# Optimization experiments

Hardware: AMD Instinct MI355X
Metric: run time of the kernel (lower is better)

The kernel has to match this reference:

```python
import jax, jax.numpy as jnp
import numpy as np

N, K, F, H, C = 16384, 16, 3, 64, 10


def setup_inputs() -> dict:
    key = jax.random.key(0)
    ks = jax.random.split(key, 6)
    pos = jax.random.normal(ks[0], (N, F), jnp.float32)
    batch = jnp.zeros((N,), jnp.int32)  # single graph
    W1 = jax.random.normal(ks[1], (2 * F, H), jnp.float32) * 0.1
    b1 = jnp.zeros((H,), jnp.float32)
    W2 = jax.random.normal(ks[2], (2 * H, H), jnp.float32) * 0.1
    b2 = jnp.zeros((H,), jnp.float32)
    Wc = jax.random.normal(ks[3], (H, C), jnp.float32) * 0.1
    bc = jnp.zeros((C,), jnp.float32)
    return {"pos": pos, "batch": batch, "W1": W1, "b1": b1,
            "W2": W2, "b2": b2, "Wc": Wc, "bc": bc}


def knn_graph(pos, k):
    # brute-force knn with self-loops (loop=True): self has distance 0
    sq = jnp.sum(pos * pos, axis=1)
    d = sq[:, None] + sq[None, :] - 2.0 * (pos @ pos.T)  # [N, N]
    _, idx = jax.lax.top_k(-d, k)  # [N, k] nearest neighbor indices (incl. self)
    return idx


def edge_conv(x, idx, W, b):
    # message for edge j->i: Linear(concat(x_i, x_j - x_i)); aggregate by max over neighbors
    n, k = idx.shape
    xi = x[:, None, :]               # [N, 1, F]
    xj = x[idx]                      # [N, k, F]
    msg = jnp.concatenate([jnp.broadcast_to(xi, (n, k, x.shape[1])), xj - xi], axis=-1)
    m = msg @ W + b                  # [N, k, H]
    return jnp.max(m, axis=1)        # [N, H]


def reference(pos, batch, W1, b1, W2, b2, Wc, bc):
    idx = knn_graph(pos, K)
    h = jax.nn.relu(edge_conv(pos, idx, W1, b1))
    h = jax.nn.relu(edge_conv(h, idx, W2, b2))
    g = jax.ops.segment_max(h, batch, num_segments=1)  # global max pool -> [1, H]
    return g @ Wc + bc
```

## Files before the change

kernel.cpp:

```cpp
#include <hip/hip_runtime.h>

#define NPTS 16384
#define KNN 16
#define HID 64
#define NCLS 10

#define QPB 8
#define QPW 2
#define SCAP 128

__device__ __forceinline__ float distf(float4 q, float4 p) {
    float dot = fmaf(q.x, p.x, fmaf(q.y, p.y, q.z * p.z));
    return fmaf(-2.f, dot, p.w);
}

__device__ __forceinline__ unsigned long long dkey(float v, int j) {
    unsigned u = __float_as_uint(v);
    u = (u & 0x80000000u) ? ~u : (u | 0x80000000u);
    return ((unsigned long long)u << 32) | (unsigned)j;
}

__device__ __forceinline__ unsigned long long shfl_xor_u64(unsigned long long x, int m) {
    unsigned hi = (unsigned)__shfl_xor((int)(x >> 32), m, 64);
    unsigned lo = (unsigned)__shfl_xor((int)(x & 0xffffffffu), m, 64);
    return ((unsigned long long)hi << 32) | lo;
}

__device__ __forceinline__ void wave_top16_16(unsigned long long (&key)[16], int lane,
                                              int q, int* __restrict__ idx) {
    int outj = 0x7fffffff;
    for (int r = 0; r < 16; ++r) {
        unsigned long long gm = key[0];
#pragma unroll
        for (int s = 1; s < 16; ++s) gm = key[s] < gm ? key[s] : gm;
#pragma unroll
        for (int st = 1; st < 64; st <<= 1) {
            unsigned long long o = shfl_xor_u64(gm, st);
            gm = o < gm ? o : gm;
        }
        if (lane == r) outj = (int)(gm & 0xffffffffu);
#pragma unroll
        for (int s = 0; s < 16; ++s)
            if (key[s] == gm) key[s] = ~0ull;
    }
    if (lane < 16) idx[q * KNN + lane] = outj;
}

__global__ void prep_kernel(const float* __restrict__ pos, float4* __restrict__ pos4) {
    int i = blockIdx.x * 256 + threadIdx.x;
    if (i < NPTS) {
        float x = pos[3 * i], y = pos[3 * i + 1], z = pos[3 * i + 2];
        pos4[i] = make_float4(x, y, z, fmaf(x, x, fmaf(y, y, z * z)));
    }
}

__global__ __launch_bounds__(256) void knn_kernel(const float4* __restrict__ pos4,
                                                  int* __restrict__ idx) {
    __shared__ float4 tile[256];
    __shared__ unsigned long long keys[QPB][SCAP];
    __shared__ int knt[QPB];
    int tid = threadIdx.x;
    int lane = tid & 63;
    int w = tid >> 6;
    int qb = blockIdx.x * QPB + w * QPW;
    float4 q0 = pos4[qb + 0], q1 = pos4[qb + 1];

    float m0 = INFINITY, m1 = INFINITY;
    for (int tb = 0; tb < NPTS; tb += 256) {
        __syncthreads();
        tile[tid] = pos4[tb + tid];
        __syncthreads();
#pragma unroll
        for (int r = 0; r < 4; ++r) {
            float4 p = tile[r * 64 + lane];
            m0 = fminf(m0, distf(q0, p));
            m1 = fminf(m1, distf(q1, p));
        }
    }
    m0 = fminf(m0, __shfl_xor(m0, 16, 64));
    m1 = fminf(m1, __shfl_xor(m1, 16, 64));
    m0 = fminf(m0, __shfl_xor(m0, 32, 64));
    m1 = fminf(m1, __shfl_xor(m1, 32, 64));
#pragma unroll
    for (int mk = 1; mk <= 8; mk <<= 1) {
        m0 = fmaxf(m0, __shfl_xor(m0, mk, 64));
        m1 = fmaxf(m1, __shfl_xor(m1, mk, 64));
    }
    float tq0 = m0, tq1 = m1;
    if (lane < QPW) knt[w * QPW + lane] = 0;

    for (int tb = 0; tb < NPTS; tb += 256) {
        __syncthreads();
        tile[tid] = pos4[tb + tid];
        __syncthreads();
#pragma unroll
        for (int r = 0; r < 4; ++r) {
            int jj = r * 64 + lane;
            float4 p = tile[jj];
            int j = tb + jj;
            float v0 = distf(q0, p);
            float v1 = distf(q1, p);
            if (v0 <= tq0) { int s = atomicAdd(&knt[w * QPW + 0], 1); if (s < SCAP) keys[w * QPW + 0][s] = dkey(v0, j); }
            if (v1 <= tq1) { int s = atomicAdd(&knt[w * QPW + 1], 1); if (s < SCAP) keys[w * QPW + 1][s] = dkey(v1, j); }
        }
    }

#pragma unroll
    for (int qi = 0; qi < QPW; ++qi) {
        int q = qb + qi;
        int ntot = knt[w * QPW + qi];
        if (ntot <= SCAP) {
            unsigned long long k0 = (lane < ntot) ? keys[w * QPW + qi][lane] : ~0ull;
            unsigned long long k1 = (lane + 64 < ntot) ? keys[w * QPW + qi][lane + 64] : ~0ull;
            int r0 = 0, r1 = 0;
            for (int t = 0; t < ntot; ++t) {
                unsigned long long k = keys[w * QPW + qi][t];
                r0 += (int)(k < k0);
                r1 += (int)(k < k1);
            }
            if (lane < ntot && r0 < KNN) idx[q * KNN + r0] = (int)(k0 & 0xffffffffu);
            if (lane + 64 < ntot && r1 < KNN) idx[q * KNN + r1] = (int)(k1 & 0xffffffffu);
        } else {
            float tq = (qi == 0) ? tq0 : tq1;
            float4 qq = pos4[q];
            unsigned long long key[16];
#pragma unroll
            for (int u = 0; u < 16; ++u) key[u] = ~0ull;
            for (int j = lane; j < NPTS; j += 64) {
                float v = distf(qq, pos4[j]);
                unsigned long long k = dkey(v, j);
                if (v <= tq && k < key[15]) {
#pragma unroll
                    for (int s = 0; s < 16; ++s) {
                        unsigned long long mn = k < key[s] ? k : key[s];
                        unsigned long long mx = k < key[s] ? key[s] : k;
                        key[s] = mn;
                        k = mx;
                    }
                }
            }
            wave_top16_16(key, lane, q, idx);
        }
    }
}


__global__ __launch_bounds__(256) void ec1_pre_kernel(const float4* __restrict__ pos4,
                                                      const float* __restrict__ W1,
                                                      const float* __restrict__ b1,
                                                      float* __restrict__ C1,
                                                      float* __restrict__ Y1) {
    int t = threadIdx.x & 63;
    int p = blockIdx.x * 4 + (threadIdx.x >> 6);
    float4 x = pos4[p];
    float w0 = W1[0 * HID + t], w1 = W1[1 * HID + t], w2 = W1[2 * HID + t];
    float v0 = W1[3 * HID + t], v1 = W1[4 * HID + t], v2 = W1[5 * HID + t];
    float y = fmaf(x.x, v0, fmaf(x.y, v1, x.z * v2));
    float cc = b1[t] + x.x * (w0 - v0) + x.y * (w1 - v1) + x.z * (w2 - v2);
    Y1[p * HID + t] = y;
    C1[p * HID + t] = cc;
}

__global__ __launch_bounds__(256) void ec1_max_kernel(const float* __restrict__ C1,
                                                      const float* __restrict__ Y1,
                                                      const int* __restrict__ idx,
                                                      float* __restrict__ h1) {
    int t = threadIdx.x & 63;
    int p = blockIdx.x * 4 + (threadIdx.x >> 6);
    float m = -INFINITY;
#pragma unroll
    for (int k = 0; k < KNN; ++k) {
        int j = idx[p * KNN + k];
        m = fmaxf(m, Y1[j * HID + t]);
    }
    h1[p * HID + t] = fmaxf(C1[p * HID + t] + m, 0.f);
}

__global__ __launch_bounds__(256) void ec2_pre_kernel(const float* __restrict__ h1,
                                                      const float* __restrict__ W2,
                                                      const float* __restrict__ b2,
                                                      float* __restrict__ C2,
                                                      float* __restrict__ Y2) {
    int t = threadIdx.x & 63;
    int r = threadIdx.x >> 6;
    int pb = blockIdx.x * 16 + r * 4;
    float aa[4] = {0.f, 0.f, 0.f, 0.f};
    float ab[4] = {0.f, 0.f, 0.f, 0.f};
#pragma unroll 8
    for (int f = 0; f < 64; ++f) {
        float wa = W2[f * HID + t];
        float wb = W2[(64 + f) * HID + t];
#pragma unroll
        for (int i = 0; i < 4; ++i) {
            float h = h1[(pb + i) * HID + f];
            aa[i] = fmaf(h, wa, aa[i]);
            ab[i] = fmaf(h, wb, ab[i]);
        }
    }
    float bt = b2[t];
#pragma unroll
    for (int i = 0; i < 4; ++i) {
        C2[(pb + i) * HID + t] = bt + aa[i] - ab[i];
        Y2[(pb + i) * HID + t] = ab[i];
    }
}

__global__ __launch_bounds__(256) void ec2_maxpool_kernel(const float* __restrict__ C2,
                                                          const float* __restrict__ Y2,
                                                          const int* __restrict__ idx,
                                                          float* __restrict__ gpartial) {
    int t = threadIdx.x & 63;
    int lp = threadIdx.x >> 6;
    int p = blockIdx.x * 4 + lp;
    float m = -INFINITY;
#pragma unroll
    for (int k = 0; k < KNN; ++k) {
        int j = idx[p * KNN + k];
        m = fmaxf(m, Y2[j * HID + t]);
    }
    float val = fmaxf(C2[p * HID + t] + m, 0.f);
    __shared__ float red[4][64];
    red[lp][t] = val;
    __syncthreads();
    if (lp == 0) {
        float g = fmaxf(fmaxf(red[0][t], red[1][t]), fmaxf(red[2][t], red[3][t]));
        gpartial[blockIdx.x * 64 + t] = g;
    }
}

__global__ __launch_bounds__(256) void greduce2_kernel(const float* __restrict__ gpartial,
                                                       float* __restrict__ gp2) {
    __shared__ float red[4][64];
    int f = threadIdx.x & 63;
    int w = threadIdx.x >> 6;
    int r0 = blockIdx.x * 16 + w * 4;
    float m = -INFINITY;
#pragma unroll
    for (int r = 0; r < 4; ++r) m = fmaxf(m, gpartial[(r0 + r) * 64 + f]);
    red[w][f] = m;
    __syncthreads();
    if (w == 0)
        gp2[blockIdx.x * 64 + f] =
            fmaxf(fmaxf(red[0][f], red[1][f]), fmaxf(red[2][f], red[3][f]));
}

__global__ __launch_bounds__(256) void tail2_kernel(const float* __restrict__ gp2,
                                                    const float* __restrict__ Wc,
                                                    const float* __restrict__ bc,
                                                    float* __restrict__ out) {
    __shared__ float red[4][64];
    __shared__ float g[64];
    int f = threadIdx.x & 63;
    int w = threadIdx.x >> 6;
    float m = -INFINITY;
    for (int i = w; i < 256; i += 4) m = fmaxf(m, gp2[i * 64 + f]);
    red[w][f] = m;
    __syncthreads();
    if (w == 0) g[f] = fmaxf(fmaxf(red[0][f], red[1][f]), fmaxf(red[2][f], red[3][f]));
    __syncthreads();
    if (threadIdx.x < NCLS) {
        float a = bc[threadIdx.x];
#pragma unroll
        for (int h = 0; h < HID; ++h) a = fmaf(g[h], Wc[h * NCLS + threadIdx.x], a);
        out[threadIdx.x] = a;
    }
}

extern "C" void kernel_launch(void* const* d_in, const int* in_sizes, int n_in,
                              void* d_out, int out_size, void* d_ws, size_t ws_size,
                              hipStream_t stream) {
    const float* pos = (const float*)d_in[0];
    const float* W1 = (const float*)d_in[2];
    const float* b1 = (const float*)d_in[3];
    const float* W2 = (const float*)d_in[4];
    const float* b2 = (const float*)d_in[5];
    const float* Wc = (const float*)d_in[6];
    const float* bc = (const float*)d_in[7];
    float* out = (float*)d_out;

    char* ws = (char*)d_ws;
    size_t o = 0;
    auto alloc = [&](size_t bytes) { size_t r = o; o += (bytes + 255) & ~size_t(255); return r; };
    size_t fm = (size_t)NPTS * HID * 4;
    size_t o_pos4 = alloc((size_t)NPTS * 16);
    size_t o_idx = alloc((size_t)NPTS * KNN * 4);
    size_t o_h1 = alloc(fm);
    size_t o_C1 = alloc(fm);
    size_t o_Y1 = alloc(fm);
    size_t o_C2 = alloc(fm);
    size_t o_Y2 = alloc(fm);
    size_t o_gp = alloc((size_t)(NPTS / 4) * HID * 4);
    size_t o_gp2 = alloc((size_t)256 * HID * 4);

    float4* pos4 = (float4*)(ws + o_pos4);
    int* idx = (int*)(ws + o_idx);
    float* h1 = (float*)(ws + o_h1);
    float* C1 = (float*)(ws + o_C1);
    float* Y1 = (float*)(ws + o_Y1);
    float* C2 = (float*)(ws + o_C2);
    float* Y2 = (float*)(ws + o_Y2);
    float* gp = (float*)(ws + o_gp);
    float* gp2 = (float*)(ws + o_gp2);

    prep_kernel<<<NPTS / 256, 256, 0, stream>>>(pos, pos4);
    knn_kernel<<<NPTS / QPB, 256, 0, stream>>>(pos4, idx);
    ec1_pre_kernel<<<NPTS / 4, 256, 0, stream>>>(pos4, W1, b1, C1, Y1);
    ec1_max_kernel<<<NPTS / 4, 256, 0, stream>>>(C1, Y1, idx, h1);
    ec2_pre_kernel<<<NPTS / 16, 256, 0, stream>>>(h1, W2, b2, C2, Y2);
    ec2_maxpool_kernel<<<NPTS / 4, 256, 0, stream>>>(C2, Y2, idx, gp);
    greduce2_kernel<<<256, 256, 0, stream>>>(gp, gp2);
    tail2_kernel<<<1, 256, 0, stream>>>(gp2, Wc, bc, out);
}
```

Baseline: 362.5 us.

## Raise kNN queries per wave to eight and fuse edge-conv1 pre/max kernels

The kNN kernel now gives each wave 8 query points instead of 2 and drops the shared-memory tile with its block barriers. Candidates are read straight from global memory (L2/L1 cached), so each loaded candidate is reused across more queries in registers. Separately, the first edge-conv's precompute and max kernels are merged: neighbor projections are recomputed from pos4 instead of writing and re-reading Y1/C1 buffers. Costs are higher register pressure, fewer blocks (512) for the kNN grid, and more shared-memory atomic contention per wave.

```diff
diff --git a/kernel.cpp b/kernel.cpp
--- a/kernel.cpp
+++ b/kernel.cpp
@@ -5,8 +5,8 @@
 #define HID 64
 #define NCLS 10
 
-#define QPB 8
-#define QPW 2
+#define QPW 8
+#define QPB 32
 #define SCAP 128
 
 __device__ __forceinline__ float distf(float4 q, float4 p) {
@@ -56,86 +56,88 @@
 
 __global__ __launch_bounds__(256) void knn_kernel(const float4* __restrict__ pos4,
                                                   int* __restrict__ idx) {
-    __shared__ float4 tile[256];
     __shared__ unsigned long long keys[QPB][SCAP];
     __shared__ int knt[QPB];
     int tid = threadIdx.x;
     int lane = tid & 63;
     int w = tid >> 6;
-    int qb = blockIdx.x * QPB + w * QPW;
-    float4 q0 = pos4[qb + 0], q1 = pos4[qb + 1];
-
-    float m0 = INFINITY, m1 = INFINITY;
-    for (int tb = 0; tb < NPTS; tb += 256) {
-        __syncthreads();
-        tile[tid] = pos4[tb + tid];
-        __syncthreads();
-#pragma unroll
-        for (int r = 0; r < 4; ++r) {
-            float4 p = tile[r * 64 + lane];
-            m0 = fminf(m0, distf(q0, p));
-            m1 = fminf(m1, distf(q1, p));
-        }
-    }
-    m0 = fminf(m0, __shfl_xor(m0, 16, 64));
-    m1 = fminf(m1, __shfl_xor(m1, 16, 64));
-    m0 = fminf(m0, __shfl_xor(m0, 32, 64));
-    m1 = fminf(m1, __shfl_xor(m1, 32, 64));
-#pragma unroll
-    for (int mk = 1; mk <= 8; mk <<= 1) {
-        m0 = fmaxf(m0, __shfl_xor(m0, mk, 64));
-        m1 = fmaxf(m1, __shfl_xor(m1, mk, 64));
-    }
-    float tq0 = m0, tq1 = m1;
-    if (lane < QPW) knt[w * QPW + lane] = 0;
-
-    for (int tb = 0; tb < NPTS; tb += 256) {
-        __syncthreads();
-        tile[tid] = pos4[tb + tid];
-        __syncthreads();
-#pragma unroll
-        for (int r = 0; r < 4; ++r) {
-            int jj = r * 64 + lane;
-            float4 p = tile[jj];
-            int j = tb + jj;
-            float v0 = distf(q0, p);
-            float v1 = distf(q1, p);
-            if (v0 <= tq0) { int s = atomicAdd(&knt[w * QPW + 0], 1); if (s < SCAP) keys[w * QPW + 0][s] = dkey(v0, j); }
-            if (v1 <= tq1) { int s = atomicAdd(&knt[w * QPW + 1], 1); if (s < SCAP) keys[w * QPW + 1][s] = dkey(v1, j); }
+    int w8 = w * QPW;
+    int qb = blockIdx.x * QPB + w8;
+    float4 qf[QPW];
+#pragma unroll
+    for (int i = 0; i < QPW; ++i) qf[i] = pos4[qb + i];
+
+    float mn[QPW];
+#pragma unroll
+    for (int i = 0; i < QPW; ++i) mn[i] = INFINITY;
+    for (int cb = 0; cb < NPTS; cb += 128) {
+        float4 c0 = pos4[cb + lane];
+        float4 c1 = pos4[cb + 64 + lane];
+#pragma unroll
+        for (int i = 0; i < QPW; ++i) mn[i] = fminf(mn[i], distf(qf[i], c0));
+#pragma unroll
+        for (int i = 0; i < QPW; ++i) mn[i] = fminf(mn[i], distf(qf[i], c1));
+    }
+    float tq[QPW];
+#pragma unroll
+    for (int i = 0; i < QPW; ++i) {
+        float m = mn[i];
+        m = fminf(m, __shfl_xor(m, 16, 64));
+        m = fminf(m, __shfl_xor(m, 32, 64));
+        m = fmaxf(m, __shfl_xor(m, 1, 64));
+        m = fmaxf(m, __shfl_xor(m, 2, 64));
+        m = fmaxf(m, __shfl_xor(m, 4, 64));
+        m = fmaxf(m, __shfl_xor(m, 8, 64));
+        tq[i] = m;
+    }
+    if (lane < QPW) knt[w8 + lane] = 0;
+
+    for (int cb = 0; cb < NPTS; cb += 128) {
+        float4 c0 = pos4[cb + lane];
+        float4 c1 = pos4[cb + 64 + lane];
+        int j0 = cb + lane, j1 = cb + 64 + lane;
+#pragma unroll
+        for (int i = 0; i < QPW; ++i) {
+            float v = distf(qf[i], c0);
+            if (v <= tq[i]) { int s = atomicAdd(&knt[w8 + i], 1); if (s < SCAP) keys[w8 + i][s] = dkey(v, j0); }
+        }
+#pragma unroll
+        for (int i = 0; i < QPW; ++i) {
+            float v = distf(qf[i], c1);
+            if (v <= tq[i]) { int s = atomicAdd(&knt[w8 + i], 1); if (s < SCAP) keys[w8 + i][s] = dkey(v, j1); }
         }
     }
 
 #pragma unroll
     for (int qi = 0; qi < QPW; ++qi) {
         int q = qb + qi;
-        int ntot = knt[w * QPW + qi];
+        int ntot = knt[w8 + qi];
         if (ntot <= SCAP) {
-            unsigned long long k0 = (lane < ntot) ? keys[w * QPW + qi][lane] : ~0ull;
-            unsigned long long k1 = (lane + 64 < ntot) ? keys[w * QPW + qi][lane + 64] : ~0ull;
+            unsigned long long k0 = (lane < ntot) ? keys[w8 + qi][lane] : ~0ull;
+            unsigned long long k1 = (lane + 64 < ntot) ? keys[w8 + qi][lane + 64] : ~0ull;
             int r0 = 0, r1 = 0;
             for (int t = 0; t < ntot; ++t) {
-                unsigned long long k = keys[w * QPW + qi][t];
+                unsigned long long k = keys[w8 + qi][t];
                 r0 += (int)(k < k0);
                 r1 += (int)(k < k1);
             }
             if (lane < ntot && r0 < KNN) idx[q * KNN + r0] = (int)(k0 & 0xffffffffu);
             if (lane + 64 < ntot && r1 < KNN) idx[q * KNN + r1] = (int)(k1 & 0xffffffffu);
         } else {
-            float tq = (qi == 0) ? tq0 : tq1;
-            float4 qq = pos4[q];
+            float tqq = tq[qi];
             unsigned long long key[16];
 #pragma unroll
             for (int u = 0; u < 16; ++u) key[u] = ~0ull;
             for (int j = lane; j < NPTS; j += 64) {
-                float v = distf(qq, pos4[j]);
+                float v = distf(qf[qi], pos4[j]);
                 unsigned long long k = dkey(v, j);
-                if (v <= tq && k < key[15]) {
+                if (v <= tqq && k < key[15]) {
 #pragma unroll
                     for (int s = 0; s < 16; ++s) {
-                        unsigned long long mn = k < key[s] ? k : key[s];
-                        unsigned long long mx = k < key[s] ? key[s] : k;
-                        key[s] = mn;
-                        k = mx;
+                        unsigned long long a = k < key[s] ? k : key[s];
+                        unsigned long long b = k < key[s] ? key[s] : k;
+                        key[s] = a;
+                        k = b;
                     }
                 }
             }
@@ -144,36 +146,26 @@
     }
 }
 
-
-__global__ __launch_bounds__(256) void ec1_pre_kernel(const float4* __restrict__ pos4,
-                                                      const float* __restrict__ W1,
-                                                      const float* __restrict__ b1,
-                                                      float* __restrict__ C1,
-                                                      float* __restrict__ Y1) {
+__global__ __launch_bounds__(256) void ec1_kernel(const float4* __restrict__ pos4,
+                                                  const int* __restrict__ idx,
+                                                  const float* __restrict__ W1,
+                                                  const float* __restrict__ b1,
+                                                  float* __restrict__ h1) {
     int t = threadIdx.x & 63;
     int p = blockIdx.x * 4 + (threadIdx.x >> 6);
-    float4 x = pos4[p];
+    float4 xi = pos4[p];
     float w0 = W1[0 * HID + t], w1 = W1[1 * HID + t], w2 = W1[2 * HID + t];
     float v0 = W1[3 * HID + t], v1 = W1[4 * HID + t], v2 = W1[5 * HID + t];
-    float y = fmaf(x.x, v0, fmaf(x.y, v1, x.z * v2));
-    float cc = b1[t] + x.x * (w0 - v0) + x.y * (w1 - v1) + x.z * (w2 - v2);
-    Y1[p * HID + t] = y;
-    C1[p * HID + t] = cc;
-}
-
-__global__ __launch_bounds__(256) void ec1_max_kernel(const float* __restrict__ C1,
-                                                      const float* __restrict__ Y1,
-                                                      const int* __restrict__ idx,
-                                                      float* __restrict__ h1) {
-    int t = threadIdx.x & 63;
-    int p = blockIdx.x * 4 + (threadIdx.x >> 6);
+    float C = b1[t] + xi.x * (w0 - v0) + xi.y * (w1 - v1) + xi.z * (w2 - v2);
     float m = -INFINITY;
 #pragma unroll
     for (int k = 0; k < KNN; ++k) {
         int j = idx[p * KNN + k];
-        m = fmaxf(m, Y1[j * HID + t]);
-    }
-    h1[p * HID + t] = fmaxf(C1[p * HID + t] + m, 0.f);
+        float4 xj = pos4[j];
+        float y = fmaf(xj.x, v0, fmaf(xj.y, v1, xj.z * v2));
+        m = fmaxf(m, y);
+    }
+    h1[p * HID + t] = fmaxf(C + m, 0.f);
 }
 
 __global__ __launch_bounds__(256) void ec2_pre_kernel(const float* __restrict__ h1,
@@ -285,8 +277,6 @@
     size_t o_pos4 = alloc((size_t)NPTS * 16);
     size_t o_idx = alloc((size_t)NPTS * KNN * 4);
     size_t o_h1 = alloc(fm);
-    size_t o_C1 = alloc(fm);
-    size_t o_Y1 = alloc(fm);
     size_t o_C2 = alloc(fm);
     size_t o_Y2 = alloc(fm);
     size_t o_gp = alloc((size_t)(NPTS / 4) * HID * 4);
@@ -295,8 +285,6 @@
     float4* pos4 = (float4*)(ws + o_pos4);
     int* idx = (int*)(ws + o_idx);
     float* h1 = (float*)(ws + o_h1);
-    float* C1 = (float*)(ws + o_C1);
-    float* Y1 = (float*)(ws + o_Y1);
     float* C2 = (float*)(ws + o_C2);
     float* Y2 = (float*)(ws + o_Y2);
     float* gp = (float*)(ws + o_gp);
@@ -304,8 +292,7 @@
 
     prep_kernel<<<NPTS / 256, 256, 0, stream>>>(pos, pos4);
     knn_kernel<<<NPTS / QPB, 256, 0, stream>>>(pos4, idx);
-    ec1_pre_kernel<<<NPTS / 4, 256, 0, stream>>>(pos4, W1, b1, C1, Y1);
-    ec1_max_kernel<<<NPTS / 4, 256, 0, stream>>>(C1, Y1, idx, h1);
+    ec1_kernel<<<NPTS / 4, 256, 0, stream>>>(pos4, idx, W1, b1, h1);
     ec2_pre_kernel<<<NPTS / 16, 256, 0, stream>>>(h1, W2, b2, C2, Y2);
     ec2_maxpool_kernel<<<NPTS / 4, 256, 0, stream>>>(C2, Y2, idx, gp);
     greduce2_kernel<<<256, 256, 0, stream>>>(gp, gp2);
```

Measured after the change: 380.4 us. 1.05x slower.
